# Kernel optimization log

Measured on AMD Instinct MI355X. Metric: run time of the kernel, lower is better.

## Reference

```python
import jax, jax.numpy as jnp
import numpy as np

N_GRAPHS = 256
EPS = 1e-5


def _bn(x, g, b):
    # training-mode BatchNorm1d: biased batch statistics
    m = jnp.mean(x, axis=0)
    v = jnp.mean((x - m) ** 2, axis=0)
    return (x - m) * jax.lax.rsqrt(v + EPS) * g + b


def _gcn_conv(x, W, b, src, dst, dinv, n_nodes):
    # GCNConv: D^{-1/2} (A + I) D^{-1/2} X W + b
    h = x @ W  # [N, H]
    coef = dinv[src] * dinv[dst]  # [E]
    msg = h[src] * coef[:, None]  # [E, H]
    agg = jax.ops.segment_sum(msg, dst, num_segments=n_nodes)
    agg = agg + h * (dinv * dinv)[:, None]  # self-loop term
    return agg + b


def setup_inputs() -> dict:
    key = jax.random.key(0)
    ks = jax.random.split(key, 20)
    N, E, D, H, C = 50000, 600000, 128, 128, 10
    L = 3  # num_conv_layers
    x = jax.random.normal(ks[0], (N, D), dtype=jnp.float32)
    edge_index = jax.random.randint(ks[1], (2, E), 0, N, dtype=jnp.int64)
    batch = jnp.sort(jax.random.randint(ks[2], (N,), 0, N_GRAPHS, dtype=jnp.int64))

    def xavier(k, shape):
        fan_in, fan_out = shape[0], shape[1]
        lim = float(np.sqrt(6.0 / (fan_in + fan_out)))
        return jax.random.uniform(k, shape, jnp.float32, -lim, lim)

    return {
        "x": x,
        "edge_index": edge_index,
        "batch": batch,
        "bn_feat_g": jnp.ones((D,), jnp.float32),
        "bn_feat_b": jnp.full((D,), 1e-4, jnp.float32),
        "conv_feat_W": xavier(ks[3], (D, H)),
        "conv_feat_b": jnp.zeros((H,), jnp.float32),
        "conv_W": jnp.stack([xavier(ks[4 + i], (H, H)) for i in range(L)]),
        "conv_b": jnp.zeros((L, H), jnp.float32),
        "bn_conv_g": jnp.ones((L, H), jnp.float32),
        "bn_conv_b": jnp.full((L, H), 1e-4, jnp.float32),
        "gate_W1": xavier(ks[8], (H, H)),
        "gate_b1": jnp.zeros((H,), jnp.float32),
        "gate_W2": xavier(ks[9], (H, 1)),
        "gate_b2": jnp.zeros((1,), jnp.float32),
        "fc_W": xavier(ks[10], (H, H)),
        "fc_b": jnp.zeros((H,), jnp.float32),
        "bn_fc_g": jnp.ones((H,), jnp.float32),
        "bn_fc_b": jnp.full((H,), 1e-4, jnp.float32),
        "cls_W": xavier(ks[11], (H, C)),
        "cls_b": jnp.zeros((C,), jnp.float32),
    }


def reference(x, edge_index, batch, bn_feat_g, bn_feat_b, conv_feat_W, conv_feat_b,
              conv_W, conv_b, bn_conv_g, bn_conv_b, gate_W1, gate_b1, gate_W2,
              gate_b2, fc_W, fc_b, bn_fc_g, bn_fc_b, cls_W, cls_b):
    N = x.shape[0]
    src, dst = edge_index[0], edge_index[1]
    # degree incl. self-loop (edge weights = 1)
    deg = jax.ops.segment_sum(jnp.ones_like(src, dtype=x.dtype), dst, num_segments=N) + 1.0
    dinv = jax.lax.rsqrt(deg)

    h = _bn(x, bn_feat_g, bn_feat_b)
    h = jax.nn.relu(_gcn_conv(h, conv_feat_W, conv_feat_b, src, dst, dinv, N))
    for i in range(conv_W.shape[0]):
        h = jax.nn.relu(_gcn_conv(_bn(h, bn_conv_g[i], bn_conv_b[i]),
                                  conv_W[i], conv_b[i], src, dst, dinv, N))
    gate = jax.nn.sigmoid(jax.nn.relu(h @ gate_W1 + gate_b1) @ gate_W2 + gate_b2)  # [N,1]
    g = jax.ops.segment_sum(h * gate, batch, num_segments=N_GRAPHS)  # [G, H]
    g = jax.nn.relu(_bn(g, bn_fc_g, bn_fc_b) @ fc_W + fc_b)
    logits = g @ cls_W + cls_b
    return jax.nn.log_softmax(logits, axis=-1)
```

## Files before the change

kernel.cpp:

```cpp
#include <hip/hip_runtime.h>
#include <hip/hip_fp16.h>

typedef unsigned short u16;
typedef unsigned int u32;
typedef __attribute__((ext_vector_type(8))) short short8;
typedef __attribute__((ext_vector_type(4))) float floatx4;

#define EPSI 1e-5f

__device__ __forceinline__ float b2f(u16 h) { return __uint_as_float(((u32)h) << 16); }
__device__ __forceinline__ u16 f2b(float f) {
    u32 u = __float_as_uint(f);
    return (u16)((u + 0x7fffu + ((u >> 16) & 1u)) >> 16);
}
__device__ __forceinline__ u32 pack2(float a, float b) {
    return (u32)f2b(a) | ((u32)f2b(b) << 16);
}
__device__ __forceinline__ float ldf(const void* p, int i, int fm) {
    if (fm == 1) return b2f(((const u16*)p)[i]);
    if (fm == 2) return __half2float(__ushort_as_half(((const u16*)p)[i]));
    return ((const float*)p)[i];
}
__device__ __forceinline__ int ldi(const void* p, int i, int im) {
    return im ? ((const int*)p)[2 * i] : ((const int*)p)[i];
}

__global__ void init_kernel(u32* zp, int nz, const void* ones, const void* ei, int* flags) {
    int i = blockIdx.x * 256 + threadIdx.x;
    if (i < nz) zp[i] = 0;
    if (blockIdx.x == 0 && threadIdx.x == 0) {
        u32 w = ((const u32*)ones)[0];
        int fm = 0;
        if (w == 0x3F803F80u) fm = 1;
        else if (w == 0x3C003C00u) fm = 2;
        const u32* e = (const u32*)ei;
        int all0 = 1;
        for (int k = 0; k < 16; ++k)
            if (e[2 * k + 1] != 0u) all0 = 0;
        flags[0] = fm;
        flags[1] = all0;
    }
}

__global__ void bigprep_kernel(const void* __restrict__ ei, int* __restrict__ cnt, int E,
                               const void* __restrict__ batch, int* __restrict__ bounds, int N,
                               int EB, const void* __restrict__ x, u32* __restrict__ A2,
                               float* __restrict__ stats0, const void* __restrict__ gW1,
                               const void* __restrict__ gb1, u16* __restrict__ Wtg,
                               float* __restrict__ bias2g, const void* __restrict__ cfW,
                               const void* __restrict__ cW, u16* __restrict__ Wt4,
                               const void* __restrict__ fcW, float* __restrict__ fcWf,
                               const void* __restrict__ clsW, float* __restrict__ clsWf,
                               const void* __restrict__ fcb, float* __restrict__ fcbf,
                               const void* __restrict__ clsb, float* __restrict__ clsbf,
                               const void* __restrict__ gW2, float* __restrict__ gW2f,
                               const void* __restrict__ gb2, float* __restrict__ gb2f,
                               const void* __restrict__ cfb, const void* __restrict__ cvb,
                               float* __restrict__ biasf, const int* __restrict__ flags) {
    int fm = flags[0];
    int bid = blockIdx.x, t = threadIdx.x;
    if (bid < EB) {
        int im = flags[1];
        int g = bid * 256 + t;
        if (g < E) atomicAdd(&cnt[ldi(ei, E + g, im)], 1);
        if (g < N) {
            int b = ldi(batch, g, im);
            if (g == 0) {
                for (int q = 0; q <= b; ++q) bounds[q] = 0;
            } else {
                int bp = ldi(batch, g - 1, im);
                for (int q = bp + 1; q <= b; ++q) bounds[q] = g;
            }
            if (g == N - 1) {
                for (int q = b + 1; q <= 256; ++q) bounds[q] = N;
            }
        }
        return;
    }
    int pid = bid - EB;
    if (pid < 1024) {
        int np = N * 64;
        float s0 = 0.f, s1 = 0.f, q0 = 0.f, q1 = 0.f;
        if (fm == 1) {
            const u32* xs = (const u32*)x;
            for (int j = pid * 256 + t; j < np; j += 1024 * 256) {
                u32 w = xs[j];
                A2[j] = w;
                float v0 = b2f((u16)w), v1 = b2f((u16)(w >> 16));
                s0 += v0;
                q0 += v0 * v0;
                s1 += v1;
                q1 += v1 * v1;
            }
        } else {
            for (int j = pid * 256 + t; j < np; j += 1024 * 256) {
                float v0 = ldf(x, 2 * j, fm);
                float v1 = ldf(x, 2 * j + 1, fm);
                A2[j] = pack2(v0, v1);
                s0 += v0;
                q0 += v0 * v0;
                s1 += v1;
                q1 += v1 * v1;
            }
        }
        __shared__ float2 sh[256];
        sh[t] = make_float2(s0, s1);
        __syncthreads();
        float* so = stats0 + (pid & 15) * 256;
        if (t < 64) {
            float a = 0.f, b = 0.f;
#pragma unroll
            for (int w = 0; w < 4; ++w) {
                float2 v = sh[t + w * 64];
                a += v.x;
                b += v.y;
            }
            atomicAdd(&so[2 * t], a);
            atomicAdd(&so[2 * t + 1], b);
        }
        __syncthreads();
        sh[t] = make_float2(q0, q1);
        __syncthreads();
        if (t < 64) {
            float a = 0.f, b = 0.f;
#pragma unroll
            for (int w = 0; w < 4; ++w) {
                float2 v = sh[t + w * 64];
                a += v.x;
                b += v.y;
            }
            atomicAdd(&so[128 + 2 * t], a);
            atomicAdd(&so[128 + 2 * t + 1], b);
        }
    } else if (pid < 1152) {
        int n = pid - 1024;
        if (t < 128) Wtg[n * 128 + t] = f2b(ldf(gW1, t * 128 + n, fm));
        if (t == 0) bias2g[n] = ldf(gb1, n, fm);
    } else if (pid < 1216) {
        int task = pid - 1152;
        int mat = task >> 4, tile = task & 15;
        int tr = (tile >> 2) * 32, tc = (tile & 3) * 32;
        const void* src = mat == 0 ? cfW : cW;
        int soff = mat == 0 ? 0 : (mat - 1) * 16384;
        __shared__ float tb[32][33];
#pragma unroll
        for (int i = 0; i < 4; ++i) {
            int o = t * 4 + i;
            int r = o >> 5, c = o & 31;
            tb[r][c] = ldf(src, soff + (tr + r) * 128 + tc + c, fm);
        }
        __syncthreads();
        u16* dst = Wt4 + mat * 16384;
#pragma unroll
        for (int i = 0; i < 4; ++i) {
            int o = t * 4 + i;
            int nr = o >> 5, kc = o & 31;
            dst[(tc + nr) * 128 + tr + kc] = f2b(tb[kc][nr]);
        }
    } else if (pid < 1224) {
        int base = (pid - 1216) * 2048;
        for (int i = t; i < 2048; i += 256) fcWf[base + i] = ldf(fcW, base + i, fm);
    } else {
        for (int i = t; i < 1280; i += 256) clsWf[i] = ldf(clsW, i, fm);
        for (int i = t; i < 512; i += 256)
            biasf[i] = (i < 128) ? ldf(cfb, i, fm) : ldf(cvb, i - 128, fm);
        if (t < 128) {
            fcbf[t] = ldf(fcb, t, fm);
            gW2f[t] = ldf(gW2, t, fm);
        }
        if (t < 10) clsbf[t] = ldf(clsb, t, fm);
        if (t == 0) gb2f[0] = ldf(gb2, 0, fm);
    }
}

__global__ void scan_kernel(const int* __restrict__ cnt, int* __restrict__ row_start, int n) {
    int b = blockIdx.x, t = threadIdx.x;
    __shared__ int sh[256];
    const int4* c4 = (const int4*)cnt;
    int lim4 = b * 256;
    int acc = 0;
    for (int i = t; i < lim4; i += 256) {
        int4 v = c4[i];
        acc += v.x + v.y + v.z + v.w;
    }
    sh[t] = acc;
    __syncthreads();
    for (int o = 128; o > 0; o >>= 1) {
        if (t < o) sh[t] += sh[t + o];
        __syncthreads();
    }
    int pre = sh[0];
    __syncthreads();
    int base = b * 1024 + t * 4;
    int v[4];
    int s = 0;
#pragma unroll
    for (int j = 0; j < 4; ++j) {
        int idx = base + j;
        v[j] = (idx < n) ? cnt[idx] : 0;
        s += v[j];
    }
    sh[t] = s;
    __syncthreads();
    for (int o = 1; o < 256; o <<= 1) {
        int add = (t >= o) ? sh[t - o] : 0;
        __syncthreads();
        sh[t] += add;
        __syncthreads();
    }
    int run = pre + sh[t] - s;
#pragma unroll
    for (int j = 0; j < 4; ++j) {
        int idx = base + j;
        run += v[j];
        if (idx < n) row_start[idx + 1] = run;
    }
    if (b == 0 && t == 0) row_start[0] = 0;
}

__global__ __launch_bounds__(256) void mfma_fill_kernel(
    const u16* __restrict__ A, const u16* __restrict__ Wt, const float* __restrict__ stats,
    const void* __restrict__ bng, const void* __restrict__ bnb, u16* __restrict__ C, int N,
    int mmgrid, const void* __restrict__ ei, const int* __restrict__ row_start,
    int* __restrict__ fill_cnt, const int* __restrict__ cnt, int2* __restrict__ edges, int E,
    const int* __restrict__ flags) {
    int t = threadIdx.x;
    if ((int)blockIdx.x >= mmgrid) {
        int im = flags[1];
        int e = (blockIdx.x - mmgrid) * 256 + t;
        if (e < E) {
            int s = ldi(ei, e, im);
            int d = ldi(ei, E + e, im);
            int p = row_start[d] + atomicAdd(&fill_cnt[d], 1);
            float cf = rsqrtf((float)cnt[s] + 1.0f) * rsqrtf((float)cnt[d] + 1.0f);
            edges[p] = make_int2(s, __float_as_int(cf));
        }
        return;
    }
    int fm = flags[0];
    __shared__ float scs[128], shs[128];
    if (t < 128) {
        float ms = 0.f, qs = 0.f;
#pragma unroll
        for (int c = 0; c < 16; ++c) {
            ms += stats[c * 256 + t];
            qs += stats[c * 256 + 128 + t];
        }
        float m = ms / (float)N;
        float var = qs / (float)N - m * m;
        float rs = rsqrtf(var + EPSI);
        float sc = rs * ldf(bng, t, fm);
        scs[t] = sc;
        shs[t] = ldf(bnb, t, fm) - m * sc;
    }
    __syncthreads();
    int wid = t >> 6, lane = t & 63;
    int m16 = lane & 15, q = lane >> 4;
    int row0 = blockIdx.x * 64 + wid * 16;
    if (row0 >= N) return;
    int arow = row0 + m16;
    floatx4 acc[8];
#pragma unroll
    for (int i = 0; i < 8; ++i) acc[i] = (floatx4){0.f, 0.f, 0.f, 0.f};
#pragma unroll
    for (int kc = 0; kc < 4; ++kc) {
        short8 af;
        if (arow < N) {
            short8 raw = *(const short8*)&A[(size_t)arow * 128 + kc * 32 + q * 8];
            int k0 = kc * 32 + q * 8;
#pragma unroll
            for (int j = 0; j < 8; ++j)
                af[j] = (short)f2b(b2f((u16)raw[j]) * scs[k0 + j] + shs[k0 + j]);
        } else {
#pragma unroll
            for (int j = 0; j < 8; ++j) af[j] = 0;
        }
#pragma unroll
        for (int nt = 0; nt < 8; ++nt) {
            short8 bf = *(const short8*)&Wt[(nt * 16 + m16) * 128 + kc * 32 + q * 8];
            acc[nt] = __builtin_amdgcn_mfma_f32_16x16x32_bf16(af, bf, acc[nt], 0, 0, 0);
        }
    }
#pragma unroll
    for (int nt = 0; nt < 8; ++nt) {
#pragma unroll
        for (int reg = 0; reg < 4; ++reg) {
            int r = row0 + q * 4 + reg;
            if (r < N) C[(size_t)r * 128 + nt * 16 + m16] = f2b(acc[nt][reg]);
        }
    }
}

__global__ __launch_bounds__(256) void mfma_mm_kernel(
    const u16* __restrict__ A, const u16* __restrict__ Wt, const float* __restrict__ stats,
    const void* __restrict__ bng, const void* __restrict__ bnb, int poff,
    const float* __restrict__ bias2, u16* __restrict__ C, float* __restrict__ gate,
    const float* __restrict__ gW2f, const float* __restrict__ gb2f, int N, int mode,
    const int* __restrict__ flags) {
    int t = threadIdx.x;
    __shared__ float scs[128], shs[128];
    if (stats && t < 128) {
        int fm = flags[0];
        float ms = 0.f, qs = 0.f;
#pragma unroll
        for (int c = 0; c < 16; ++c) {
            ms += stats[c * 256 + t];
            qs += stats[c * 256 + 128 + t];
        }
        float m = ms / (float)N;
        float var = qs / (float)N - m * m;
        float rs = rsqrtf(var + EPSI);
        float sc = rs * ldf(bng, poff + t, fm);
        scs[t] = sc;
        shs[t] = ldf(bnb, poff + t, fm) - m * sc;
    }
    __syncthreads();
    int wid = t >> 6, lane = t & 63;
    int m16 = lane & 15, q = lane >> 4;
    int row0 = blockIdx.x * 64 + wid * 16;
    if (row0 >= N) return;
    int arow = row0 + m16;
    floatx4 acc[8];
#pragma unroll
    for (int i = 0; i < 8; ++i) acc[i] = (floatx4){0.f, 0.f, 0.f, 0.f};
#pragma unroll
    for (int kc = 0; kc < 4; ++kc) {
        short8 af;
        if (arow < N) {
            if (stats) {
                short8 raw = *(const short8*)&A[(size_t)arow * 128 + kc * 32 + q * 8];
                int k0 = kc * 32 + q * 8;
#pragma unroll
                for (int j = 0; j < 8; ++j)
                    af[j] = (short)f2b(b2f((u16)raw[j]) * scs[k0 + j] + shs[k0 + j]);
            } else {
                af = *(const short8*)&A[(size_t)arow * 128 + kc * 32 + q * 8];
            }
        } else {
#pragma unroll
            for (int j = 0; j < 8; ++j) af[j] = 0;
        }
#pragma unroll
        for (int nt = 0; nt < 8; ++nt) {
            short8 bf = *(const short8*)&Wt[(nt * 16 + m16) * 128 + kc * 32 + q * 8];
            acc[nt] = __builtin_amdgcn_mfma_f32_16x16x32_bf16(af, bf, acc[nt], 0, 0, 0);
        }
    }
    if (mode == 0) {
#pragma unroll
        for (int nt = 0; nt < 8; ++nt) {
#pragma unroll
            for (int reg = 0; reg < 4; ++reg) {
                int r = row0 + q * 4 + reg;
                if (r < N) C[(size_t)r * 128 + nt * 16 + m16] = f2b(acc[nt][reg]);
            }
        }
    } else {
        float p[4] = {0.f, 0.f, 0.f, 0.f};
#pragma unroll
        for (int nt = 0; nt < 8; ++nt) {
            float b2v = bias2[nt * 16 + m16];
            float w2v = gW2f[nt * 16 + m16];
#pragma unroll
            for (int reg = 0; reg < 4; ++reg)
                p[reg] += fmaxf(acc[nt][reg] + b2v, 0.0f) * w2v;
        }
        float gb = gb2f[0];
#pragma unroll
        for (int reg = 0; reg < 4; ++reg) {
            float v = p[reg];
            v += __shfl_xor(v, 1);
            v += __shfl_xor(v, 2);
            v += __shfl_xor(v, 4);
            v += __shfl_xor(v, 8);
            if (m16 == 0) {
                int r = row0 + q * 4 + reg;
                if (r < N) gate[r] = 1.0f / (1.0f + expf(-(v + gb)));
            }
        }
    }
}

#define ACC1(AX, AY, V, W)                        \
    do {                                          \
        AX += b2f((u16)(V)) * (W);                \
        AY += b2f((u16)((V) >> 16)) * (W);        \
    } while (0)

__global__ __launch_bounds__(512) void agg_kernel(
    const u32* __restrict__ C2, const int* __restrict__ row_start,
    const int2* __restrict__ edges, const float* __restrict__ biasf, int boff,
    u32* __restrict__ A2, float* __restrict__ statsOut, int N) {
    int t = threadIdx.x;
    int wid = t >> 6, lane = t & 63;
    int n0 = blockIdx.x * 16 + wid;
    int n1 = n0 + 8;
    float ax0 = 0.f, ay0 = 0.f, ax1 = 0.f, ay1 = 0.f;
    int rs0 = 0, re0 = 0, rs1 = 0, re1 = 0;
    if (n0 < N) {
        rs0 = row_start[n0];
        re0 = row_start[n0 + 1];
        float d2 = 1.0f / ((float)(re0 - rs0) + 1.0f);
        u32 s = C2[(size_t)n0 * 64 + lane];
        ax0 = b2f((u16)s) * d2;
        ay0 = b2f((u16)(s >> 16)) * d2;
    }
    if (n1 < N) {
        rs1 = row_start[n1];
        re1 = row_start[n1 + 1];
        float d2 = 1.0f / ((float)(re1 - rs1) + 1.0f);
        u32 s = C2[(size_t)n1 * 64 + lane];
        ax1 = b2f((u16)s) * d2;
        ay1 = b2f((u16)(s >> 16)) * d2;
    }
    int e0 = rs0, e1 = rs1;
    while (e0 + 4 <= re0 && e1 + 4 <= re1) {
        int2 ea[4], eb[4];
        u32 va[4], vb[4];
#pragma unroll
        for (int j = 0; j < 4; ++j) {
            ea[j] = edges[e0 + j];
            eb[j] = edges[e1 + j];
        }
#pragma unroll
        for (int j = 0; j < 4; ++j) {
            va[j] = C2[(size_t)ea[j].x * 64 + lane];
            vb[j] = C2[(size_t)eb[j].x * 64 + lane];
        }
#pragma unroll
        for (int j = 0; j < 4; ++j) {
            ACC1(ax0, ay0, va[j], __int_as_float(ea[j].y));
            ACC1(ax1, ay1, vb[j], __int_as_float(eb[j].y));
        }
        e0 += 4;
        e1 += 4;
    }
    for (; e0 + 4 <= re0; e0 += 4) {
        int2 ed[4];
        u32 vi[4];
#pragma unroll
        for (int j = 0; j < 4; ++j) ed[j] = edges[e0 + j];
#pragma unroll
        for (int j = 0; j < 4; ++j) vi[j] = C2[(size_t)ed[j].x * 64 + lane];
#pragma unroll
        for (int j = 0; j < 4; ++j) ACC1(ax0, ay0, vi[j], __int_as_float(ed[j].y));
    }
    for (; e0 < re0; ++e0) {
        int2 ed = edges[e0];
        u32 v = C2[(size_t)ed.x * 64 + lane];
        ACC1(ax0, ay0, v, __int_as_float(ed.y));
    }
    for (; e1 + 4 <= re1; e1 += 4) {
        int2 ed[4];
        u32 vi[4];
#pragma unroll
        for (int j = 0; j < 4; ++j) ed[j] = edges[e1 + j];
#pragma unroll
        for (int j = 0; j < 4; ++j) vi[j] = C2[(size_t)ed[j].x * 64 + lane];
#pragma unroll
        for (int j = 0; j < 4; ++j) ACC1(ax1, ay1, vi[j], __int_as_float(ed[j].y));
    }
    for (; e1 < re1; ++e1) {
        int2 ed = edges[e1];
        u32 v = C2[(size_t)ed.x * 64 + lane];
        ACC1(ax1, ay1, v, __int_as_float(ed.y));
    }
    float2 bv = ((const float2*)(biasf + boff))[lane];
    if (n0 < N) {
        ax0 = fmaxf(ax0 + bv.x, 0.0f);
        ay0 = fmaxf(ay0 + bv.y, 0.0f);
        A2[(size_t)n0 * 64 + lane] = pack2(ax0, ay0);
    }
    if (n1 < N) {
        ax1 = fmaxf(ax1 + bv.x, 0.0f);
        ay1 = fmaxf(ay1 + bv.y, 0.0f);
        A2[(size_t)n1 * 64 + lane] = pack2(ax1, ay1);
    }
    if (!statsOut) return;
    __shared__ float2 sh[512];
    sh[t] = make_float2(ax0 + ax1, ay0 + ay1);
    __syncthreads();
    float* so = statsOut + (blockIdx.x & 15) * 256;
    if (t < 64) {
        float a = 0.f, b = 0.f;
#pragma unroll
        for (int w = 0; w < 8; ++w) {
            float2 v = sh[t + w * 64];
            a += v.x;
            b += v.y;
        }
        atomicAdd(&so[2 * t], a);
        atomicAdd(&so[2 * t + 1], b);
    }
    __syncthreads();
    sh[t] = make_float2(ax0 * ax0 + ax1 * ax1, ay0 * ay0 + ay1 * ay1);
    __syncthreads();
    if (t < 64) {
        float a = 0.f, b = 0.f;
#pragma unroll
        for (int w = 0; w < 8; ++w) {
            float2 v = sh[t + w * 64];
            a += v.x;
            b += v.y;
        }
        atomicAdd(&so[128 + 2 * t], a);
        atomicAdd(&so[128 + 2 * t + 1], b);
    }
}

__global__ void pool_kernel(const u16* __restrict__ A, const float* __restrict__ gate,
                            const int* __restrict__ bounds, float* __restrict__ pooled,
                            float* __restrict__ statsP) {
    int g = blockIdx.x;
    int t = threadIdx.x;
    int f = t & 127, half = t >> 7;
    int s = bounds[g], e = bounds[g + 1];
    float acc = 0.f;
    for (int r = s + half; r < e; r += 2) acc += b2f(A[(size_t)r * 128 + f]) * gate[r];
    __shared__ float sh[256];
    sh[t] = acc;
    __syncthreads();
    if (t < 128) {
        float v = sh[t] + sh[t + 128];
        pooled[g * 128 + t] = v;
        float* so = statsP + (g & 7) * 256;
        atomicAdd(&so[t], v);
        atomicAdd(&so[128 + t], v * v);
    }
}

__global__ __launch_bounds__(256) void fc_cls_kernel(
    const float* __restrict__ pooled, const float* __restrict__ statsP,
    const void* __restrict__ bng, const void* __restrict__ bnb,
    const float* __restrict__ fcWf, const float* __restrict__ fcbf,
    const float* __restrict__ clsWf, const float* __restrict__ clsbf, void* __restrict__ out,
    const int* __restrict__ flags) {
    int fm = flags[0];
    int g = blockIdx.x, t = threadIdx.x;
    __shared__ float pv[128];
    __shared__ float red[256];
    __shared__ float fco[128];
    __shared__ float lg[10];
    __shared__ float redv[2];
    if (t < 128) {
        float ms = 0.f, qs = 0.f;
#pragma unroll
        for (int c = 0; c < 8; ++c) {
            ms += statsP[c * 256 + t];
            qs += statsP[c * 256 + 128 + t];
        }
        float m = ms / 256.0f;
        float var = qs / 256.0f - m * m;
        float rs = rsqrtf(var + EPSI);
        float sc = rs * ldf(bng, t, fm);
        pv[t] = pooled[g * 128 + t] * sc + (ldf(bnb, t, fm) - m * sc);
    }
    __syncthreads();
    {
        int j = t & 127, half = t >> 7;
        float acc = 0.f;
        int k0 = half * 64;
#pragma unroll 8
        for (int k = k0; k < k0 + 64; ++k) acc += pv[k] * fcWf[k * 128 + j];
        red[t] = acc;
    }
    __syncthreads();
    if (t < 128) fco[t] = fmaxf(red[t] + red[t + 128] + fcbf[t], 0.0f);
    __syncthreads();
    if (t < 10) {
        float a = clsbf[t];
#pragma unroll 8
        for (int k = 0; k < 128; ++k) a += fco[k] * clsWf[k * 10 + t];
        lg[t] = a;
    }
    __syncthreads();
    if (t == 0) {
        float mx = lg[0];
        for (int j = 1; j < 10; ++j) mx = fmaxf(mx, lg[j]);
        float se = 0.f;
        for (int j = 0; j < 10; ++j) se += expf(lg[j] - mx);
        redv[0] = mx;
        redv[1] = logf(se);
    }
    __syncthreads();
    if (t < 10) {
        float v = lg[t] - redv[0] - redv[1];
        if (fm == 1) ((u16*)out)[g * 10 + t] = f2b(v);
        else if (fm == 2) ((u16*)out)[g * 10 + t] = __half_as_ushort(__float2half(v));
        else ((float*)out)[g * 10 + t] = v;
    }
}

extern "C" void kernel_launch(void* const* d_in, const int* in_sizes, int n_in,
                              void* d_out, int out_size, void* d_ws, size_t ws_size,
                              hipStream_t stream) {
    const void* x = d_in[0];
    const void* ei = d_in[1];
    const void* batch = d_in[2];
    const void* bn_feat_g = d_in[3];
    const void* bn_feat_b = d_in[4];
    const void* conv_feat_W = d_in[5];
    const void* conv_feat_b = d_in[6];
    const void* conv_W = d_in[7];
    const void* conv_b = d_in[8];
    const void* bn_conv_g = d_in[9];
    const void* bn_conv_b = d_in[10];
    const void* gate_W1 = d_in[11];
    const void* gate_b1 = d_in[12];
    const void* gate_W2 = d_in[13];
    const void* gate_b2 = d_in[14];
    const void* fc_W = d_in[15];
    const void* fc_b = d_in[16];
    const void* bn_fc_g = d_in[17];
    const void* bn_fc_b = d_in[18];
    const void* cls_W = d_in[19];
    const void* cls_b = d_in[20];

    const int N = in_sizes[2];
    const int E = in_sizes[1] / 2;
    const int NB = (N + 1023) / 1024;
    const int EB = ((E > N ? E : N) + 255) / 256;

    u32* ws = (u32*)d_ws;
    size_t off = 0;
    auto alloc = [&](size_t n) {
        size_t o = off;
        off += (n + 63) & ~(size_t)63;
        return o;
    };
    size_t o_cnt = alloc(N);
    size_t o_fill = alloc(N);
    size_t o_stats = alloc(5 * 4096);
    size_t o_statsP = alloc(2048);
    size_t zero_end = off;
    size_t o_flags = alloc(16);
    size_t o_rs = alloc((size_t)N + 1);
    size_t o_edges = alloc((size_t)E * 2);
    size_t o_wtg = alloc(128 * 128 / 2);
    size_t o_b2g = alloc(128);
    size_t o_Wt4 = alloc(4 * 16384 / 2);
    size_t o_fcW = alloc(16384);
    size_t o_fcb = alloc(128);
    size_t o_clsW = alloc(1280);
    size_t o_clsb = alloc(16);
    size_t o_gW2 = alloc(128);
    size_t o_gb2 = alloc(16);
    size_t o_biasf = alloc(512);
    size_t o_gate = alloc(N);
    size_t o_bnd = alloc(257);
    size_t o_pool = alloc(256 * 128);
    size_t o_A = alloc((size_t)N * 64);
    size_t o_C = alloc((size_t)N * 64);
    (void)ws_size;
    (void)n_in;
    (void)out_size;

    int* cnt = (int*)(ws + o_cnt);
    int* fillc = (int*)(ws + o_fill);
    float* stats = (float*)(ws + o_stats);
    float* statsP = (float*)(ws + o_statsP);
    int* flags = (int*)(ws + o_flags);
    int* row_start = (int*)(ws + o_rs);
    int2* edges = (int2*)(ws + o_edges);
    u16* Wtg = (u16*)(ws + o_wtg);
    float* bias2g = (float*)(ws + o_b2g);
    u16* Wt4 = (u16*)(ws + o_Wt4);
    float* fcWf = (float*)(ws + o_fcW);
    float* fcbf = (float*)(ws + o_fcb);
    float* clsWf = (float*)(ws + o_clsW);
    float* clsbf = (float*)(ws + o_clsb);
    float* gW2f = (float*)(ws + o_gW2);
    float* gb2f = (float*)(ws + o_gb2);
    float* biasf = (float*)(ws + o_biasf);
    float* gateb = (float*)(ws + o_gate);
    int* bnd = (int*)(ws + o_bnd);
    float* pooled = (float*)(ws + o_pool);
    u16* A = (u16*)(ws + o_A);
    u16* C = (u16*)(ws + o_C);

    int nz = (int)zero_end;
    init_kernel<<<(nz + 255) / 256, 256, 0, stream>>>(ws, nz, bn_feat_g, ei, flags);
    bigprep_kernel<<<EB + 1225, 256, 0, stream>>>(
        ei, cnt, E, batch, bnd, N, EB, x, (u32*)A, stats, gate_W1, gate_b1, Wtg, bias2g,
        conv_feat_W, conv_W, Wt4, fc_W, fcWf, cls_W, clsWf, fc_b, fcbf, cls_b, clsbf, gate_W2,
        gW2f, gate_b2, gb2f, conv_feat_b, conv_b, biasf, flags);
    scan_kernel<<<NB, 256, 0, stream>>>(cnt, row_start, N);

    int mmgrid = (N + 63) / 64;
    int agggrid = (N + 15) / 16;
    mfma_fill_kernel<<<mmgrid + EB, 256, 0, stream>>>(A, Wt4, stats, bn_feat_g, bn_feat_b, C, N,
                                                      mmgrid, ei, row_start, fillc, cnt, edges,
                                                      E, flags);
    for (int l = 0; l < 4; ++l) {
        if (l > 0)
            mfma_mm_kernel<<<mmgrid, 256, 0, stream>>>(
                A, Wt4 + (size_t)l * 16384, stats + (size_t)l * 4096, bn_conv_g, bn_conv_b,
                (l - 1) * 128, nullptr, C, nullptr, nullptr, nullptr, N, 0, flags);
        float* so = (l < 3) ? stats + (size_t)(l + 1) * 4096 : nullptr;
        agg_kernel<<<agggrid, 512, 0, stream>>>((const u32*)C, row_start, edges, biasf, l * 128,
                                                (u32*)A, so, N);
    }

    mfma_mm_kernel<<<mmgrid, 256, 0, stream>>>(A, Wtg, nullptr, nullptr, nullptr, 0, bias2g,
                                               nullptr, gateb, gW2f, gb2f, N, 2, flags);
    pool_kernel<<<256, 256, 0, stream>>>(A, gateb, bnd, pooled, statsP);
    fc_cls_kernel<<<256, 256, 0, stream>>>(pooled, statsP, bn_fc_g, bn_fc_b, fcWf, fcbf, clsWf,
                                           clsbf, d_out, flags);
}
```

Baseline: 473.5 us.

## Split each node's edges across quarter-waves with 16-byte gathers in aggregation

The aggregation kernel now gives each wavefront one node instead of two. Each of its four 16-lane groups handles a different edge and fetches a full 256-byte feature row with 16-byte vector loads. Partial sums are then combined with cross-lane shuffles and exchanged through shared memory so each lane stores two features. This is meant to put more independent gathers in flight and issue fewer, wider memory requests for each edge. In exchange it adds shuffle and shared-memory overhead and wastes lanes on nodes with few edges. Separately, the pooling kernel reads packed bf16 pairs and unrolls over rows.

New measurement: 446.4 us. 5.7% less time.

```diff
diff --git a/kernel.cpp b/kernel.cpp
--- a/kernel.cpp
+++ b/kernel.cpp
@@ -23,6 +23,18 @@
 }
 __device__ __forceinline__ int ldi(const void* p, int i, int im) {
     return im ? ((const int*)p)[2 * i] : ((const int*)p)[i];
+}
+
+__device__ __forceinline__ void acc8(float* a, int4 v, float w) {
+    u32 x = (u32)v.x, y = (u32)v.y, z = (u32)v.z, q = (u32)v.w;
+    a[0] += b2f((u16)x) * w;
+    a[1] += b2f((u16)(x >> 16)) * w;
+    a[2] += b2f((u16)y) * w;
+    a[3] += b2f((u16)(y >> 16)) * w;
+    a[4] += b2f((u16)z) * w;
+    a[5] += b2f((u16)(z >> 16)) * w;
+    a[6] += b2f((u16)q) * w;
+    a[7] += b2f((u16)(q >> 16)) * w;
 }
 
 __global__ void init_kernel(u32* zp, int nz, const void* ones, const void* ei, int* flags) {
@@ -381,104 +393,62 @@
     }
 }
 
-#define ACC1(AX, AY, V, W)                        \
-    do {                                          \
-        AX += b2f((u16)(V)) * (W);                \
-        AY += b2f((u16)((V) >> 16)) * (W);        \
-    } while (0)
-
 __global__ __launch_bounds__(512) void agg_kernel(
     const u32* __restrict__ C2, const int* __restrict__ row_start,
     const int2* __restrict__ edges, const float* __restrict__ biasf, int boff,
     u32* __restrict__ A2, float* __restrict__ statsOut, int N) {
     int t = threadIdx.x;
     int wid = t >> 6, lane = t & 63;
-    int n0 = blockIdx.x * 16 + wid;
-    int n1 = n0 + 8;
-    float ax0 = 0.f, ay0 = 0.f, ax1 = 0.f, ay1 = 0.f;
-    int rs0 = 0, re0 = 0, rs1 = 0, re1 = 0;
-    if (n0 < N) {
-        rs0 = row_start[n0];
-        re0 = row_start[n0 + 1];
-        float d2 = 1.0f / ((float)(re0 - rs0) + 1.0f);
-        u32 s = C2[(size_t)n0 * 64 + lane];
-        ax0 = b2f((u16)s) * d2;
-        ay0 = b2f((u16)(s >> 16)) * d2;
-    }
-    if (n1 < N) {
-        rs1 = row_start[n1];
-        re1 = row_start[n1 + 1];
-        float d2 = 1.0f / ((float)(re1 - rs1) + 1.0f);
-        u32 s = C2[(size_t)n1 * 64 + lane];
-        ax1 = b2f((u16)s) * d2;
-        ay1 = b2f((u16)(s >> 16)) * d2;
-    }
-    int e0 = rs0, e1 = rs1;
-    while (e0 + 4 <= re0 && e1 + 4 <= re1) {
-        int2 ea[4], eb[4];
-        u32 va[4], vb[4];
-#pragma unroll
-        for (int j = 0; j < 4; ++j) {
-            ea[j] = edges[e0 + j];
-            eb[j] = edges[e1 + j];
-        }
-#pragma unroll
-        for (int j = 0; j < 4; ++j) {
-            va[j] = C2[(size_t)ea[j].x * 64 + lane];
-            vb[j] = C2[(size_t)eb[j].x * 64 + lane];
-        }
-#pragma unroll
-        for (int j = 0; j < 4; ++j) {
-            ACC1(ax0, ay0, va[j], __int_as_float(ea[j].y));
-            ACC1(ax1, ay1, vb[j], __int_as_float(eb[j].y));
-        }
-        e0 += 4;
-        e1 += 4;
-    }
-    for (; e0 + 4 <= re0; e0 += 4) {
-        int2 ed[4];
-        u32 vi[4];
-#pragma unroll
-        for (int j = 0; j < 4; ++j) ed[j] = edges[e0 + j];
-#pragma unroll
-        for (int j = 0; j < 4; ++j) vi[j] = C2[(size_t)ed[j].x * 64 + lane];
-#pragma unroll
-        for (int j = 0; j < 4; ++j) ACC1(ax0, ay0, vi[j], __int_as_float(ed[j].y));
-    }
-    for (; e0 < re0; ++e0) {
-        int2 ed = edges[e0];
-        u32 v = C2[(size_t)ed.x * 64 + lane];
-        ACC1(ax0, ay0, v, __int_as_float(ed.y));
-    }
-    for (; e1 + 4 <= re1; e1 += 4) {
-        int2 ed[4];
-        u32 vi[4];
-#pragma unroll
-        for (int j = 0; j < 4; ++j) ed[j] = edges[e1 + j];
-#pragma unroll
-        for (int j = 0; j < 4; ++j) vi[j] = C2[(size_t)ed[j].x * 64 + lane];
-#pragma unroll
-        for (int j = 0; j < 4; ++j) ACC1(ax1, ay1, vi[j], __int_as_float(ed[j].y));
-    }
-    for (; e1 < re1; ++e1) {
-        int2 ed = edges[e1];
-        u32 v = C2[(size_t)ed.x * 64 + lane];
-        ACC1(ax1, ay1, v, __int_as_float(ed.y));
-    }
-    float2 bv = ((const float2*)(biasf + boff))[lane];
-    if (n0 < N) {
-        ax0 = fmaxf(ax0 + bv.x, 0.0f);
-        ay0 = fmaxf(ay0 + bv.y, 0.0f);
-        A2[(size_t)n0 * 64 + lane] = pack2(ax0, ay0);
-    }
-    if (n1 < N) {
-        ax1 = fmaxf(ax1 + bv.x, 0.0f);
-        ay1 = fmaxf(ay1 + bv.y, 0.0f);
-        A2[(size_t)n1 * 64 + lane] = pack2(ax1, ay1);
+    int g = lane >> 4, p = lane & 15;
+    int n = blockIdx.x * 8 + wid;
+    float acc[8];
+#pragma unroll
+    for (int j = 0; j < 8; ++j) acc[j] = 0.f;
+    if (n < N) {
+        int rs = row_start[n], re = row_start[n + 1];
+        if (g == 0) {
+            float d2 = 1.0f / ((float)(re - rs) + 1.0f);
+            int4 s = *(const int4*)&C2[(size_t)n * 64 + p * 4];
+            acc8(acc, s, d2);
+        }
+        for (int e = rs; e < re; e += 16) {
+            int iA = e + g, iB = e + 4 + g, iC = e + 8 + g, iD = e + 12 + g;
+            int2 eA = edges[iA < re ? iA : re - 1];
+            int2 eB = edges[iB < re ? iB : re - 1];
+            int2 eC = edges[iC < re ? iC : re - 1];
+            int2 eD = edges[iD < re ? iD : re - 1];
+            int4 vA = *(const int4*)&C2[(size_t)eA.x * 64 + p * 4];
+            int4 vB = *(const int4*)&C2[(size_t)eB.x * 64 + p * 4];
+            int4 vC = *(const int4*)&C2[(size_t)eC.x * 64 + p * 4];
+            int4 vD = *(const int4*)&C2[(size_t)eD.x * 64 + p * 4];
+            acc8(acc, vA, iA < re ? __int_as_float(eA.y) : 0.f);
+            acc8(acc, vB, iB < re ? __int_as_float(eB.y) : 0.f);
+            acc8(acc, vC, iC < re ? __int_as_float(eC.y) : 0.f);
+            acc8(acc, vD, iD < re ? __int_as_float(eD.y) : 0.f);
+        }
+    }
+#pragma unroll
+    for (int j = 0; j < 8; ++j) {
+        acc[j] += __shfl_xor(acc[j], 16);
+        acc[j] += __shfl_xor(acc[j], 32);
+    }
+    __shared__ float xch[8][128];
+    if (g == 0) {
+#pragma unroll
+        for (int j = 0; j < 8; ++j) xch[wid][p * 8 + j] = acc[j];
+    }
+    __syncthreads();
+    float ax = 0.f, ay = 0.f;
+    if (n < N) {
+        float2 bv = ((const float2*)(biasf + boff))[lane];
+        float2 v = ((const float2*)xch[wid])[lane];
+        ax = fmaxf(v.x + bv.x, 0.0f);
+        ay = fmaxf(v.y + bv.y, 0.0f);
+        A2[(size_t)n * 64 + lane] = pack2(ax, ay);
     }
     if (!statsOut) return;
     __shared__ float2 sh[512];
-    sh[t] = make_float2(ax0 + ax1, ay0 + ay1);
+    sh[t] = make_float2(ax, ay);
     __syncthreads();
     float* so = statsOut + (blockIdx.x & 15) * 256;
     if (t < 64) {
@@ -493,7 +463,7 @@
         atomicAdd(&so[2 * t + 1], b);
     }
     __syncthreads();
-    sh[t] = make_float2(ax0 * ax0 + ax1 * ax1, ay0 * ay0 + ay1 * ay1);
+    sh[t] = make_float2(ax * ax, ay * ay);
     __syncthreads();
     if (t < 64) {
         float a = 0.f, b = 0.f;
@@ -508,24 +478,43 @@
     }
 }
 
-__global__ void pool_kernel(const u16* __restrict__ A, const float* __restrict__ gate,
+__global__ void pool_kernel(const u32* __restrict__ A2, const float* __restrict__ gate,
                             const int* __restrict__ bounds, float* __restrict__ pooled,
                             float* __restrict__ statsP) {
     int g = blockIdx.x;
     int t = threadIdx.x;
-    int f = t & 127, half = t >> 7;
+    int f2 = t & 63, grp = t >> 6;
     int s = bounds[g], e = bounds[g + 1];
-    float acc = 0.f;
-    for (int r = s + half; r < e; r += 2) acc += b2f(A[(size_t)r * 128 + f]) * gate[r];
-    __shared__ float sh[256];
-    sh[t] = acc;
-    __syncthreads();
-    if (t < 128) {
-        float v = sh[t] + sh[t + 128];
-        pooled[g * 128 + t] = v;
+    float ax = 0.f, ay = 0.f;
+    int r = s + grp;
+    for (; r + 4 < e; r += 8) {
+        u32 v0 = A2[(size_t)r * 64 + f2];
+        u32 v1 = A2[(size_t)(r + 4) * 64 + f2];
+        float g0 = gate[r], g1 = gate[r + 4];
+        ax += b2f((u16)v0) * g0;
+        ay += b2f((u16)(v0 >> 16)) * g0;
+        ax += b2f((u16)v1) * g1;
+        ay += b2f((u16)(v1 >> 16)) * g1;
+    }
+    if (r < e) {
+        u32 v0 = A2[(size_t)r * 64 + f2];
+        float g0 = gate[r];
+        ax += b2f((u16)v0) * g0;
+        ay += b2f((u16)(v0 >> 16)) * g0;
+    }
+    __shared__ float2 sh[256];
+    sh[t] = make_float2(ax, ay);
+    __syncthreads();
+    if (t < 64) {
+        float2 a = sh[t], b = sh[t + 64], c = sh[t + 128], d = sh[t + 192];
+        float x = a.x + b.x + c.x + d.x;
+        float y = a.y + b.y + c.y + d.y;
+        ((float2*)(pooled + g * 128))[t] = make_float2(x, y);
         float* so = statsP + (g & 7) * 256;
-        atomicAdd(&so[t], v);
-        atomicAdd(&so[128 + t], v * v);
+        atomicAdd(&so[2 * t], x);
+        atomicAdd(&so[2 * t + 1], y);
+        atomicAdd(&so[128 + 2 * t], x * x);
+        atomicAdd(&so[128 + 2 * t + 1], y * y);
     }
 }
 
@@ -687,7 +676,7 @@
     scan_kernel<<<NB, 256, 0, stream>>>(cnt, row_start, N);
 
     int mmgrid = (N + 63) / 64;
-    int agggrid = (N + 15) / 16;
+    int agggrid = (N + 7) / 8;
     mfma_fill_kernel<<<mmgrid + EB, 256, 0, stream>>>(A, Wt4, stats, bn_feat_g, bn_feat_b, C, N,
                                                       mmgrid, ei, row_start, fillc, cnt, edges,
                                                       E, flags);
@@ -703,7 +692,7 @@
 
     mfma_mm_kernel<<<mmgrid, 256, 0, stream>>>(A, Wtg, nullptr, nullptr, nullptr, 0, bias2g,
                                                nullptr, gateb, gW2f, gb2f, N, 2, flags);
-    pool_kernel<<<256, 256, 0, stream>>>(A, gateb, bnd, pooled, statsP);
+    pool_kernel<<<256, 256, 0, stream>>>((const u32*)A, gateb, bnd, pooled, statsP);
     fc_cls_kernel<<<256, 256, 0, stream>>>(pooled, statsP, bn_fc_g, bn_fc_b, fcWf, fcbf, clsWf,
                                            clsbf, d_out, flags);
 }
```
